# Performance work log

Hardware: AMD Instinct MI355X
Metric: run time of the kernel (lower is better)

Reference implementation:

```python
import jax, jax.numpy as jnp
import numpy as np

B, T, D, H, C = 1024, 128, 13, 512, 9
EPS = 1e-5


def _layer_norm(x, g, b):
    m = x.mean(-1, keepdims=True)
    v = ((x - m) ** 2).mean(-1, keepdims=True)
    return (x - m) / jnp.sqrt(v + EPS) * g + b


def _batch_norm(x, g, b):
    # x: (B, T, H); BatchNorm1d over channel H -> stats over (B, T), biased var
    m = x.mean((0, 1))
    v = ((x - m) ** 2).mean((0, 1))
    return (x - m) / jnp.sqrt(v + EPS) * g + b


def _star_layer(x, WxK, bxK, Wxz, bxz, WhK, bhK, bn_g, bn_b):
    # Precompute input projections for all timesteps (batched GEMMs)
    xK = jnp.einsum('btd,hd->bth', x, WxK) + bxK          # (B,T,H)
    z = jnp.tanh(jnp.einsum('btd,hd->bth', x, Wxz) + bxz)  # (B,T,H)
    h0 = jnp.zeros((x.shape[0], WhK.shape[0]), x.dtype)

    def step(h, inp):
        gK, zt = inp
        K = jax.nn.sigmoid(gK + h @ WhK.T + bhK)
        hn = jnp.tanh(K * h + (1.0 - K) * zt)
        return hn, hn

    _, outs = jax.lax.scan(step, h0, (xK.swapaxes(0, 1), z.swapaxes(0, 1)))
    outs = outs.swapaxes(0, 1)  # (B,T,H)
    return _batch_norm(outs, bn_g, bn_b)


def setup_inputs() -> dict:
    key = jax.random.key(0)
    ks = jax.random.split(key, 10)

    def w(k, o, i):
        return jax.random.normal(k, (o, i), jnp.float32) / np.sqrt(i)

    return {
        'x': jax.random.normal(ks[0], (B, T, D), jnp.float32),
        'inln_g': jnp.ones((D,), jnp.float32),
        'inln_b': jnp.zeros((D,), jnp.float32),
        # layer 1 (input_dim -> H)
        'WxK1': w(ks[1], H, D), 'bxK1': jnp.ones((H,), jnp.float32),
        'Wxz1': w(ks[2], H, D), 'bxz1': jnp.zeros((H,), jnp.float32),
        'WhK1': w(ks[3], H, H), 'bhK1': jnp.zeros((H,), jnp.float32),
        'bn1_g': jnp.ones((H,), jnp.float32), 'bn1_b': jnp.zeros((H,), jnp.float32),
        # layer 2 == layer 3 (shared module instance in the original Sequential)
        'WxK2': w(ks[4], H, H), 'bxK2': jnp.ones((H,), jnp.float32),
        'Wxz2': w(ks[5], H, H), 'bxz2': jnp.zeros((H,), jnp.float32),
        'WhK2': w(ks[6], H, H), 'bhK2': jnp.zeros((H,), jnp.float32),
        'bn2_g': jnp.ones((H,), jnp.float32), 'bn2_b': jnp.zeros((H,), jnp.float32),
        'cln_g': jnp.ones((H,), jnp.float32), 'cln_b': jnp.zeros((H,), jnp.float32),
        'Wc': w(ks[7], C, H), 'bc': jnp.zeros((C,), jnp.float32),
    }


def reference(x, inln_g, inln_b,
              WxK1, bxK1, Wxz1, bxz1, WhK1, bhK1, bn1_g, bn1_b,
              WxK2, bxK2, Wxz2, bxz2, WhK2, bhK2, bn2_g, bn2_b,
              cln_g, cln_b, Wc, bc):
    x = _layer_norm(x, inln_g, inln_b)
    o = _star_layer(x, WxK1, bxK1, Wxz1, bxz1, WhK1, bhK1, bn1_g, bn1_b)
    # layers 2 and 3 share the same weights and batchnorm (duplicated module)
    o = _star_layer(o, WxK2, bxK2, Wxz2, bxz2, WhK2, bhK2, bn2_g, bn2_b)
    o = _star_layer(o, WxK2, bxK2, Wxz2, bxz2, WhK2, bhK2, bn2_g, bn2_b)
    h = _layer_norm(o[:, -1, :], cln_g, cln_b)
    logits = h @ Wc.T + bc
    return jax.nn.log_softmax(logits, axis=-1)
```

## Files before the change

### kernel.cpp

```cpp
#include <hip/hip_runtime.h>
#include <hip/hip_bf16.h>
#include <math.h>

#define B_ 1024
#define T_ 128
#define D_ 13
#define H_ 512
#define C_ 9
#define TC_ 32
#define NC_ (T_/TC_)
#define NT_ (B_*T_)
#define EPS 1e-5f
#define WPAD 520

using frag_ab = __attribute__((ext_vector_type(8))) short;
using frag_cd = __attribute__((ext_vector_type(4))) float;
typedef unsigned short ushort8 __attribute__((ext_vector_type(8)));

static __device__ __forceinline__ float bf2f(unsigned short u){
  union { unsigned int i; float f; } v; v.i = ((unsigned int)u)<<16; return v.f;
}
static __device__ __forceinline__ unsigned short f2bf(float f){
  union { float f; unsigned int i; } v; v.f = f;
  unsigned int r = v.i + 0x7FFF + ((v.i >> 16) & 1);
  return (unsigned short)(r >> 16);
}
static __device__ __forceinline__ float sigmoidf_(float x){ return 1.0f/(1.0f+__expf(-x)); }
static __device__ __forceinline__ float tanhf_(float x){
  return 1.0f - 2.0f/(__expf(2.0f*x)+1.0f);
}

__global__ void k_zero(unsigned int* __restrict__ p, int n){
  int i=blockIdx.x*256+threadIdx.x; if(i<n) p[i]=0u;
}

__global__ void k_swz(const float* __restrict__ Wf, unsigned short* __restrict__ Wz){
  int dst = blockIdx.x*256 + threadIdx.x;
  int w = dst >> 15;
  int i = (dst >> 9) & 63;
  int L = (dst >> 3) & 63;
  int e = dst & 7;
  int kc = i >> 2, c = i & 3;
  int row = w*64 + c*16 + (L & 15);
  int col = kc*32 + ((L >> 4) << 3) + e;
  Wz[dst] = f2bf(Wf[row*H_ + col]);
}

__global__ __launch_bounds__(256) void k_proj1(
    const float* __restrict__ x, const float* __restrict__ g, const float* __restrict__ bvec,
    const float* __restrict__ WxK, const float* __restrict__ bxK,
    const float* __restrict__ Wxz, const float* __restrict__ bxz,
    unsigned short* __restrict__ xKo, unsigned short* __restrict__ zo, int t0)
{
  __shared__ float wK[H_*D_];
  __shared__ float wz[H_*D_];
  __shared__ float xn[TC_][D_];
  int tid = threadIdx.x;
  int b = blockIdx.x;
  const float* xin = x + ((size_t)b*T_ + t0)*D_;
  for(int i=tid;i<H_*D_;i+=256){ wK[i]=WxK[i]; wz[i]=Wxz[i]; }
  for(int i=tid;i<TC_*D_;i+=256){ ((float*)xn)[i] = xin[i]; }
  __syncthreads();
  if(tid<TC_){
    float m=0.f; for(int d=0;d<D_;++d) m+=xn[tid][d]; m*=(1.0f/D_);
    float v=0.f; for(int d=0;d<D_;++d){float t=xn[tid][d]-m; v+=t*t;} v*=(1.0f/D_);
    float inv = rsqrtf(v+EPS);
    for(int d=0;d<D_;++d) xn[tid][d] = (xn[tid][d]-m)*inv*g[d]+bvec[d];
  }
  __syncthreads();
  size_t ob = (size_t)b*TC_*H_;
  for(int hh=0; hh<2; ++hh){
    int h = tid + hh*256;
    float bK = bxK[h], bz = bxz[h];
    for(int r=0;r<TC_;++r){
      float aK=bK, az=bz;
      #pragma unroll
      for(int d=0;d<D_;++d){ float xv = xn[r][d]; aK += xv*wK[h*D_+d]; az += xv*wz[h*D_+d]; }
      xKo[ob + (size_t)r*H_ + h] = f2bf(aK);
      zo [ob + (size_t)r*H_ + h] = f2bf(tanhf_(az));
    }
  }
}

__global__ __launch_bounds__(512,2) void k_recur3(
    const unsigned short* __restrict__ xK, const unsigned short* __restrict__ z,
    const unsigned short* __restrict__ Wz,
    const float* __restrict__ bhK,
    unsigned short* __restrict__ o,
    float* __restrict__ hbuf, int t0)
{
  __shared__ __align__(16) unsigned short Wl[8*8192];
  __shared__ __align__(16) unsigned short hb[16][WPAD];
  int tid=threadIdx.x, lane=tid&63, w=tid>>6;
  int q=lane>>4, cl=lane&15;
  int b0 = blockIdx.x*16;
  for(int i=tid;i<8192;i+=512){
    int gi = i*8;
    int wv = gi>>13, off = gi&8191;
    *(ushort8*)&Wl[gi] = *(const ushort8*)&Wz[((size_t)wv<<15) + off];
  }
  float hp[16];
  float bh[4]; int col[4];
  #pragma unroll
  for(int c=0;c<4;++c){ col[c]=w*64 + c*16 + cl; bh[c]=bhK[col[c]]; }
  if(t0==0){
    for(int i=tid;i<16*H_;i+=512){ int r=i>>9,c=i&511; hb[r][c]=0; }
    #pragma unroll
    for(int i=0;i<16;++i) hp[i]=0.f;
  } else {
    for(int i=tid;i<16*H_;i+=512){ int r=i>>9,c=i&511; hb[r][c]=f2bf(hbuf[(size_t)(b0+r)*H_+c]); }
    #pragma unroll
    for(int c=0;c<4;++c)
      #pragma unroll
      for(int rg=0;rg<4;++rg) hp[c*4+rg]=hbuf[(size_t)(b0+q*4+rg)*H_+col[c]];
  }
  const unsigned short* wb = Wz + ((size_t)w<<15);
  const unsigned short* wl = Wl + w*8192;
  __syncthreads();
  for(int dt=0;dt<TC_;++dt){
    float gkv[16], zv[16];
    #pragma unroll
    for(int c=0;c<4;++c)
      #pragma unroll
      for(int rg=0;rg<4;++rg){
        size_t gi = ((size_t)(b0+q*4+rg)*TC_ + dt)*H_ + col[c];
        gkv[c*4+rg]=bf2f(xK[gi]); zv[c*4+rg]=bf2f(z[gi]);
      }
    frag_cd acc[4] = {};
    #pragma unroll
    for(int kc=0;kc<16;++kc){
      frag_ab af = *(const frag_ab*)&hb[cl][kc*32 + q*8];
      #pragma unroll
      for(int c=0;c<4;++c){
        frag_ab bf = (kc<4) ? *(const frag_ab*)&wl[(kc*4+c)*512 + lane*8]
                            : *(const frag_ab*)&wb[(kc*4+c)*512 + lane*8];
        acc[c] = __builtin_amdgcn_mfma_f32_16x16x32_bf16(af, bf, acc[c], 0,0,0);
      }
    }
    __syncthreads();
    unsigned short hnb[16];
    #pragma unroll
    for(int c=0;c<4;++c){
      #pragma unroll
      for(int rg=0;rg<4;++rg){
        int idx = c*4+rg;
        float gv = acc[c][rg] + bh[c] + gkv[idx];
        float K  = sigmoidf_(gv);
        float hn = tanhf_(K*hp[idx] + (1.f-K)*zv[idx]);
        hp[idx]=hn;
        hnb[idx]=f2bf(hn);
        hb[q*4+rg][col[c]] = hnb[idx];
      }
    }
    __syncthreads();
    #pragma unroll
    for(int c=0;c<4;++c)
      #pragma unroll
      for(int rg=0;rg<4;++rg)
        o[((size_t)(b0+q*4+rg)*T_ + t0+dt)*H_ + col[c]] = hnb[c*4+rg];
  }
  #pragma unroll
  for(int c=0;c<4;++c)
    #pragma unroll
    for(int rg=0;rg<4;++rg) hbuf[(size_t)(b0+q*4+rg)*H_+col[c]] = hp[c*4+rg];
}

__global__ __launch_bounds__(512) void k_bnstats(const unsigned short* __restrict__ o, float* __restrict__ sums){
  int c = threadIdx.x;
  int r0 = blockIdx.x*(NT_/256);
  float s=0.f, sq=0.f;
  for(int r=0;r<NT_/256;++r){
    float v = bf2f(o[(size_t)(r0+r)*H_ + c]);
    s+=v; sq+=v*v;
  }
  atomicAdd(&sums[c], s); atomicAdd(&sums[H_+c], sq);
}

__global__ void k_foldw(const float* __restrict__ WxK, const float* __restrict__ Wxz,
                        const float* __restrict__ stats, const float* __restrict__ bng,
                        unsigned short* __restrict__ Wp){
  int i = blockIdx.x*256+threadIdx.x;
  int n = i>>9, k = i&511;
  float mean = stats[k]*(1.f/NT_);
  float var  = stats[H_+k]*(1.f/NT_) - mean*mean;
  float s = bng[k]*rsqrtf(var+EPS);
  float wv = (n<H_) ? WxK[(size_t)n*H_+k] : Wxz[(size_t)(n-H_)*H_+k];
  Wp[i] = f2bf(wv*s);
}

__global__ __launch_bounds__(256) void k_foldb(const float* __restrict__ WxK, const float* __restrict__ Wxz,
                        const float* __restrict__ stats, const float* __restrict__ bng, const float* __restrict__ bnb,
                        const float* __restrict__ bxK, const float* __restrict__ bxz,
                        float* __restrict__ biasp){
  int w = threadIdx.x>>6, lane=threadIdx.x&63;
  int n = blockIdx.x*4 + w;
  const float* W = (n<H_) ? &WxK[(size_t)n*H_] : &Wxz[(size_t)(n-H_)*H_];
  float base = (n<H_) ? bxK[n] : bxz[n-H_];
  float acc=0.f;
  for(int k=lane;k<H_;k+=64){
    float mean = stats[k]*(1.f/NT_);
    float var  = stats[H_+k]*(1.f/NT_)-mean*mean;
    float s = bng[k]*rsqrtf(var+EPS);
    float t = bnb[k]-mean*s;
    acc += t*W[k];
  }
  for(int off=32;off;off>>=1) acc += __shfl_down(acc, off, 64);
  if(lane==0) biasp[n] = base + acc;
}

__global__ __launch_bounds__(256) void k_proj23(
    const unsigned short* __restrict__ A,
    const unsigned short* __restrict__ Wp,
    const float* __restrict__ biasp,
    unsigned short* __restrict__ xKo, unsigned short* __restrict__ zo, int t0)
{
  __shared__ __align__(16) unsigned short As[128*32];
  __shared__ __align__(16) unsigned short Bs[128*32];
  int tid=threadIdx.x, lane=tid&63, w=tid>>6;
  int q=lane>>4, cl=lane&15;
  int b0p = blockIdx.x*4;
  int n0 = blockIdx.y*128;
  int wm = (w>>1)*64, wn=(w&1)*64;
  frag_cd acc[4][4] = {};
  int sr = tid>>1, cb = (tid&1)*16;
  size_t arow = ((size_t)(b0p + (sr>>5))*T_ + t0 + (sr&31))*H_;
  size_t brow = (size_t)(n0+sr)*H_;
  for(int k0=0;k0<H_;k0+=32){
    *(frag_ab*)&As[sr*32+cb]   = *(const frag_ab*)&A [arow + k0+cb];
    *(frag_ab*)&As[sr*32+cb+8] = *(const frag_ab*)&A [arow + k0+cb+8];
    *(frag_ab*)&Bs[sr*32+cb]   = *(const frag_ab*)&Wp[brow + k0+cb];
    *(frag_ab*)&Bs[sr*32+cb+8] = *(const frag_ab*)&Wp[brow + k0+cb+8];
    __syncthreads();
    frag_ab af[4], bfr[4];
    #pragma unroll
    for(int mt=0;mt<4;++mt) af[mt]  = *(const frag_ab*)&As[(wm+mt*16+cl)*32 + q*8];
    #pragma unroll
    for(int nt=0;nt<4;++nt) bfr[nt] = *(const frag_ab*)&Bs[(wn+nt*16+cl)*32 + q*8];
    #pragma unroll
    for(int mt=0;mt<4;++mt)
      #pragma unroll
      for(int nt=0;nt<4;++nt)
        acc[mt][nt] = __builtin_amdgcn_mfma_f32_16x16x32_bf16(af[mt], bfr[nt], acc[mt][nt],0,0,0);
    __syncthreads();
  }
  #pragma unroll
  for(int nt=0;nt<4;++nt){
    int coln = n0+wn+nt*16+cl;
    float bp = biasp[coln];
    bool isz = coln>=H_;
    #pragma unroll
    for(int mt=0;mt<4;++mt){
      #pragma unroll
      for(int rg=0;rg<4;++rg){
        int rm = wm+mt*16+q*4+rg;
        size_t orow = (size_t)(b0p*TC_ + rm)*H_;
        float v = acc[mt][nt][rg] + bp;
        if(isz) zo [orow + coln-H_] = f2bf(tanhf_(v));
        else    xKo[orow + coln]    = f2bf(v);
      }
    }
  }
}

__global__ __launch_bounds__(512) void k_head(const unsigned short* __restrict__ o,
     const float* __restrict__ stats, const float* __restrict__ bng, const float* __restrict__ bnb,
     const float* __restrict__ clng, const float* __restrict__ clnb,
     const float* __restrict__ Wc, const float* __restrict__ bc, float* __restrict__ out)
{
  __shared__ float red[8];
  __shared__ float lred[8][9];
  int tid=threadIdx.x, lane=tid&63, w=tid>>6;
  int b = blockIdx.x;
  int c = tid;
  float v = bf2f(o[((size_t)b*T_ + (T_-1))*H_ + c]);
  float mean = stats[c]*(1.f/NT_), var = stats[H_+c]*(1.f/NT_)-mean*mean;
  float s = bng[c]*rsqrtf(var+EPS);
  float y = v*s + (bnb[c]-mean*s);
  float sm=y;
  for(int off=32;off;off>>=1) sm+=__shfl_down(sm,off,64);
  if(lane==0) red[w]=sm;
  __syncthreads();
  float mu=0.f; for(int i=0;i<8;++i) mu+=red[i]; mu*=(1.f/H_);
  float d = y-mu;
  float vq = d*d;
  for(int off=32;off;off>>=1) vq+=__shfl_down(vq,off,64);
  __syncthreads();
  if(lane==0) red[w]=vq;
  __syncthreads();
  float vv=0.f; for(int i=0;i<8;++i) vv+=red[i]; vv*=(1.f/H_);
  float yn = d*rsqrtf(vv+EPS)*clng[c]+clnb[c];
  for(int cls=0;cls<C_;++cls){
    float t = yn*Wc[(size_t)cls*H_+c];
    for(int off=32;off;off>>=1) t+=__shfl_down(t,off,64);
    if(lane==0) lred[w][cls]=t;
  }
  __syncthreads();
  if(tid==0){
    float lg[C_]; float mx=-1e30f;
    for(int cls=0;cls<C_;++cls){
      float t=bc[cls]; for(int i=0;i<8;++i) t+=lred[i][cls];
      lg[cls]=t; mx=fmaxf(mx,t);
    }
    float se=0.f; for(int cls=0;cls<C_;++cls) se+=__expf(lg[cls]-mx);
    float lse=mx+logf(se);
    for(int cls=0;cls<C_;++cls) out[(size_t)b*C_+cls]=lg[cls]-lse;
  }
}

extern "C" void kernel_launch(void* const* d_in, const int* in_sizes, int n_in,
                              void* d_out, int out_size, void* d_ws, size_t ws_size,
                              hipStream_t stream)
{
  (void)in_sizes; (void)n_in; (void)out_size; (void)ws_size;
  const float* x    =(const float*)d_in[0];
  const float* inlng=(const float*)d_in[1];
  const float* inlnb=(const float*)d_in[2];
  const float* WxK1 =(const float*)d_in[3];
  const float* bxK1 =(const float*)d_in[4];
  const float* Wxz1 =(const float*)d_in[5];
  const float* bxz1 =(const float*)d_in[6];
  const float* WhK1 =(const float*)d_in[7];
  const float* bhK1 =(const float*)d_in[8];
  const float* bn1g =(const float*)d_in[9];
  const float* bn1b =(const float*)d_in[10];
  const float* WxK2 =(const float*)d_in[11];
  const float* bxK2 =(const float*)d_in[12];
  const float* Wxz2 =(const float*)d_in[13];
  const float* bxz2 =(const float*)d_in[14];
  const float* WhK2 =(const float*)d_in[15];
  const float* bhK2 =(const float*)d_in[16];
  const float* bn2g =(const float*)d_in[17];
  const float* bn2b =(const float*)d_in[18];
  const float* clng =(const float*)d_in[19];
  const float* clnb =(const float*)d_in[20];
  const float* Wc   =(const float*)d_in[21];
  const float* bc   =(const float*)d_in[22];
  float* out=(float*)d_out;

  char* p=(char*)d_ws;
  unsigned short* o   =(unsigned short*)p; p+=(size_t)NT_*H_*2;
  unsigned short* xK  =(unsigned short*)p; p+=(size_t)B_*TC_*H_*2;
  unsigned short* z   =(unsigned short*)p; p+=(size_t)B_*TC_*H_*2;
  float* hbuf         =(float*)p;          p+=(size_t)B_*H_*4;
  unsigned short* Wz1 =(unsigned short*)p; p+=(size_t)H_*H_*2;
  unsigned short* Wz2 =(unsigned short*)p; p+=(size_t)H_*H_*2;
  unsigned short* Wp  =(unsigned short*)p; p+=(size_t)1024*H_*2;
  float* biasp        =(float*)p;          p+=1024*4;
  float* stats        =(float*)p;          p+=3*1024*4;

  k_zero<<<12,256,0,stream>>>((unsigned int*)stats, 3*1024);
  k_swz<<<H_*H_/256,256,0,stream>>>(WhK1, Wz1);
  k_swz<<<H_*H_/256,256,0,stream>>>(WhK2, Wz2);

  for(int c=0;c<NC_;++c){
    k_proj1<<<B_,256,0,stream>>>(x,inlng,inlnb,WxK1,bxK1,Wxz1,bxz1,xK,z,c*TC_);
    k_recur3<<<64,512,0,stream>>>(xK,z,Wz1,bhK1,o,hbuf,c*TC_);
  }
  k_bnstats<<<256,512,0,stream>>>(o, stats);

  k_foldw<<<1024*H_/256,256,0,stream>>>(WxK2,Wxz2,stats,bn1g,Wp);
  k_foldb<<<256,256,0,stream>>>(WxK2,Wxz2,stats,bn1g,bn1b,bxK2,bxz2,biasp);
  dim3 g23(B_/4, 8);
  for(int c=0;c<NC_;++c){
    k_proj23<<<g23,256,0,stream>>>(o,Wp,biasp,xK,z,c*TC_);
    k_recur3<<<64,512,0,stream>>>(xK,z,Wz2,bhK2,o,hbuf,c*TC_);
  }
  k_bnstats<<<256,512,0,stream>>>(o, stats+1024);

  k_foldw<<<1024*H_/256,256,0,stream>>>(WxK2,Wxz2,stats+1024,bn2g,Wp);
  k_foldb<<<256,256,0,stream>>>(WxK2,Wxz2,stats+1024,bn2g,bn2b,bxK2,bxz2,biasp);
  for(int c=0;c<NC_;++c){
    k_proj23<<<g23,256,0,stream>>>(o,Wp,biasp,xK,z,c*TC_);
    k_recur3<<<64,512,0,stream>>>(xK,z,Wz2,bhK2,o,hbuf,c*TC_);
  }
  k_bnstats<<<256,512,0,stream>>>(o, stats+2048);

  k_head<<<B_,512,0,stream>>>(o, stats+2048, bn2g,bn2b, clng,clnb, Wc,bc, out);
}
```

Before: 3.986 ms.

## Double-buffer recurrent hidden state and replace block barriers with LDS flag counter

The recurrent kernel now ping-pongs the bf16 hidden state between two shared-memory buffers. The two per-timestep __syncthreads are replaced by a workgroup-scope atomic counter: each wave increments it after its LDS writes complete, and spins until all 8 waves have finished the previous step. The aim is to let waves drift relative to each other and drop full-barrier stalls on the serial critical path. The shared weight cache is also relaid out: 15 fragments per wave live in LDS and the rest come from global memory, and launch bounds drop to one block per CU. The trade-off is spin-wait overhead and hand-rolled memory-ordering correctness in exchange for the barriers.

```diff
diff --git a/kernel.cpp b/kernel.cpp
--- a/kernel.cpp
+++ b/kernel.cpp
@@ -11,7 +11,7 @@
 #define NC_ (T_/TC_)
 #define NT_ (B_*T_)
 #define EPS 1e-5f
-#define WPAD 520
+#define LGKM_ONLY 0xc07f
 
 using frag_ab = __attribute__((ext_vector_type(8))) short;
 using frag_cd = __attribute__((ext_vector_type(4))) float;
@@ -82,42 +82,48 @@
   }
 }
 
-__global__ __launch_bounds__(512,2) void k_recur3(
+__global__ __launch_bounds__(512,1) void k_recur5(
     const unsigned short* __restrict__ xK, const unsigned short* __restrict__ z,
     const unsigned short* __restrict__ Wz,
     const float* __restrict__ bhK,
     unsigned short* __restrict__ o,
     float* __restrict__ hbuf, int t0)
 {
-  __shared__ __align__(16) unsigned short Wl[8*8192];
-  __shared__ __align__(16) unsigned short hb[16][WPAD];
+  __shared__ __align__(16) unsigned short Wl[8*15*512];
+  __shared__ __align__(16) unsigned short hbd[2][16*512];
+  __shared__ unsigned int flg;
   int tid=threadIdx.x, lane=tid&63, w=tid>>6;
   int q=lane>>4, cl=lane&15;
   int b0 = blockIdx.x*16;
-  for(int i=tid;i<8192;i+=512){
-    int gi = i*8;
-    int wv = gi>>13, off = gi&8191;
-    *(ushort8*)&Wl[gi] = *(const ushort8*)&Wz[((size_t)wv<<15) + off];
-  }
+  const unsigned short* wb = Wz + ((size_t)w<<15);
+  for(int j=tid;j<7680;j+=512){
+    int wv = j/960, off8 = j%960;
+    *(ushort8*)&Wl[wv*7680 + off8*8] = *(const ushort8*)&Wz[((size_t)wv<<15) + off8*8];
+  }
+  if(tid==0) flg = 0u;
   float hp[16];
   float bh[4]; int col[4];
   #pragma unroll
   for(int c=0;c<4;++c){ col[c]=w*64 + c*16 + cl; bh[c]=bhK[col[c]]; }
   if(t0==0){
-    for(int i=tid;i<16*H_;i+=512){ int r=i>>9,c=i&511; hb[r][c]=0; }
+    for(int i=tid;i<16*H_;i+=512) hbd[0][i]=0;
     #pragma unroll
     for(int i=0;i<16;++i) hp[i]=0.f;
   } else {
-    for(int i=tid;i<16*H_;i+=512){ int r=i>>9,c=i&511; hb[r][c]=f2bf(hbuf[(size_t)(b0+r)*H_+c]); }
+    for(int i=tid;i<16*H_;i+=512){ int r=i>>9,c=i&511; hbd[0][i]=f2bf(hbuf[(size_t)(b0+r)*H_+c]); }
     #pragma unroll
     for(int c=0;c<4;++c)
       #pragma unroll
       for(int rg=0;rg<4;++rg) hp[c*4+rg]=hbuf[(size_t)(b0+q*4+rg)*H_+col[c]];
   }
-  const unsigned short* wb = Wz + ((size_t)w<<15);
-  const unsigned short* wl = Wl + w*8192;
+  const unsigned short* wl = Wl + w*7680;
   __syncthreads();
   for(int dt=0;dt<TC_;++dt){
+    int cb = dt&1, nb = cb^1;
+    if(dt){
+      while(__hip_atomic_load(&flg, __ATOMIC_RELAXED, __HIP_MEMORY_SCOPE_WORKGROUP) < 8u*(unsigned)dt){ }
+      asm volatile("" ::: "memory");
+    }
     float gkv[16], zv[16];
     #pragma unroll
     for(int c=0;c<4;++c)
@@ -129,15 +135,15 @@
     frag_cd acc[4] = {};
     #pragma unroll
     for(int kc=0;kc<16;++kc){
-      frag_ab af = *(const frag_ab*)&hb[cl][kc*32 + q*8];
+      frag_ab af = *(const frag_ab*)&hbd[cb][cl*512 + kc*32 + q*8];
       #pragma unroll
       for(int c=0;c<4;++c){
-        frag_ab bf = (kc<4) ? *(const frag_ab*)&wl[(kc*4+c)*512 + lane*8]
-                            : *(const frag_ab*)&wb[(kc*4+c)*512 + lane*8];
+        int f = kc*4+c;
+        frag_ab bf = (f<15) ? *(const frag_ab*)&wl[f*512 + lane*8]
+                            : *(const frag_ab*)&wb[f*512 + lane*8];
         acc[c] = __builtin_amdgcn_mfma_f32_16x16x32_bf16(af, bf, acc[c], 0,0,0);
       }
     }
-    __syncthreads();
     unsigned short hnb[16];
     #pragma unroll
     for(int c=0;c<4;++c){
@@ -149,10 +155,13 @@
         float hn = tanhf_(K*hp[idx] + (1.f-K)*zv[idx]);
         hp[idx]=hn;
         hnb[idx]=f2bf(hn);
-        hb[q*4+rg][col[c]] = hnb[idx];
+        hbd[nb][(q*4+rg)*512 + col[c]] = hnb[idx];
       }
     }
-    __syncthreads();
+    asm volatile("" ::: "memory");
+    __builtin_amdgcn_s_waitcnt(LGKM_ONLY);
+    if(lane==0) __hip_atomic_fetch_add(&flg, 1u, __ATOMIC_RELAXED, __HIP_MEMORY_SCOPE_WORKGROUP);
+    asm volatile("" ::: "memory");
     #pragma unroll
     for(int c=0;c<4;++c)
       #pragma unroll
@@ -354,7 +363,7 @@
 
   for(int c=0;c<NC_;++c){
     k_proj1<<<B_,256,0,stream>>>(x,inlng,inlnb,WxK1,bxK1,Wxz1,bxz1,xK,z,c*TC_);
-    k_recur3<<<64,512,0,stream>>>(xK,z,Wz1,bhK1,o,hbuf,c*TC_);
+    k_recur5<<<64,512,0,stream>>>(xK,z,Wz1,bhK1,o,hbuf,c*TC_);
   }
   k_bnstats<<<256,512,0,stream>>>(o, stats);
 
@@ -363,7 +372,7 @@
   dim3 g23(B_/4, 8);
   for(int c=0;c<NC_;++c){
     k_proj23<<<g23,256,0,stream>>>(o,Wp,biasp,xK,z,c*TC_);
-    k_recur3<<<64,512,0,stream>>>(xK,z,Wz2,bhK2,o,hbuf,c*TC_);
+    k_recur5<<<64,512,0,stream>>>(xK,z,Wz2,bhK2,o,hbuf,c*TC_);
   }
   k_bnstats<<<256,512,0,stream>>>(o, stats+1024);
 
@@ -371,7 +380,7 @@
   k_foldb<<<256,256,0,stream>>>(WxK2,Wxz2,stats+1024,bn2g,bn2b,bxK2,bxz2,biasp);
   for(int c=0;c<NC_;++c){
     k_proj23<<<g23,256,0,stream>>>(o,Wp,biasp,xK,z,c*TC_);
-    k_recur3<<<64,512,0,stream>>>(xK,z,Wz2,bhK2,o,hbuf,c*TC_);
+    k_recur5<<<64,512,0,stream>>>(xK,z,Wz2,bhK2,o,hbuf,c*TC_);
   }
   k_bnstats<<<256,512,0,stream>>>(o, stats+2048);
 
```

Measured after the change: 5.491 ms. 1.38x slower.
